# Optimization experiments

Hardware: AMD Instinct MI355X
Metric: run time of the kernel (lower is better)

## Reference

```python
import jax, jax.numpy as jnp
import numpy as np

N = 131072        # total nodes (2048 graphs * MAX_N)
E = 1048576       # edges
F_IN = 128        # g_feature_n
INT_D = 256       # int_d
H1, C1 = 8, 8     # gl: heads, head_d
C2 = 256          # gl2: out channels, heads=1
MAX_N = 64
NEG_SLOPE = 0.2
BN_EPS = 1e-5


def _gat_conv(x, src, dst, W, att_src, att_dst, bias, heads, out_c):
    """PyG GATConv (concat=True), self-loops already appended to src/dst."""
    n = x.shape[0]
    h = (x @ W.T).reshape(n, heads, out_c)                  # [N,H,C]
    a_s = jnp.sum(h * att_src, axis=-1)                     # [N,H]
    a_d = jnp.sum(h * att_dst, axis=-1)                     # [N,H]
    alpha = jax.nn.leaky_relu(a_s[src] + a_d[dst], NEG_SLOPE)  # [E',H]
    amax = jax.ops.segment_max(alpha, dst, num_segments=n)  # stable segment softmax
    e = jnp.exp(alpha - amax[dst])
    denom = jax.ops.segment_sum(e, dst, num_segments=n)
    w = e / (denom[dst] + 1e-16)                            # [E',H]
    out = jax.ops.segment_sum(h[src] * w[..., None], dst, num_segments=n)
    return out.reshape(n, heads * out_c) + bias


def setup_inputs() -> dict:
    key = jax.random.key(0)
    ks = jax.random.split(key, 20)
    s = 0.1
    return {
        "x": jax.random.normal(ks[0], (N, F_IN), jnp.float32),
        "edge_index": jax.random.randint(ks[1], (2, E), 0, N, jnp.int64),
        # lin_embed
        "We": jax.random.normal(ks[2], (INT_D, F_IN), jnp.float32) * s,
        "be": jnp.zeros((INT_D,), jnp.float32),
        # batchnorm (eval mode, running stats)
        "bn_gamma": jnp.ones((INT_D,), jnp.float32),
        "bn_beta": jnp.zeros((INT_D,), jnp.float32),
        "bn_mean": jax.random.normal(ks[3], (INT_D,), jnp.float32) * 0.01,
        "bn_var": jax.random.uniform(ks[4], (INT_D,), jnp.float32, 0.5, 1.5),
        # gl: GATConv(INT_D -> C1, heads=H1)
        "W1": jax.random.normal(ks[5], (H1 * C1, INT_D), jnp.float32) * s,
        "as1": jax.random.normal(ks[6], (1, H1, C1), jnp.float32) * s,
        "ad1": jax.random.normal(ks[7], (1, H1, C1), jnp.float32) * s,
        "b1": jnp.zeros((H1 * C1,), jnp.float32),
        # gl2: GATConv(H1*C1 -> C2, heads=1)
        "W2": jax.random.normal(ks[8], (C2, H1 * C1), jnp.float32) * s,
        "as2": jax.random.normal(ks[9], (1, 1, C2), jnp.float32) * s,
        "ad2": jax.random.normal(ks[10], (1, 1, C2), jnp.float32) * s,
        "b2": jnp.zeros((C2,), jnp.float32),
        # lin_out
        "Wo": jax.random.normal(ks[11], (1, INT_D), jnp.float32) * s,
        "bo": jnp.zeros((1,), jnp.float32),
    }


def reference(x, edge_index, We, be, bn_gamma, bn_beta, bn_mean, bn_var,
              W1, as1, ad1, b1, W2, as2, ad2, b2, Wo, bo):
    n = x.shape[0]
    loops = jnp.arange(n)
    src = jnp.concatenate([edge_index[0], loops])  # add_self_loops=True (PyG default)
    dst = jnp.concatenate([edge_index[1], loops])

    h = x @ We.T + be
    h = (h - bn_mean) * jax.lax.rsqrt(bn_var + BN_EPS) * bn_gamma + bn_beta

    h = jax.nn.elu(_gat_conv(h, src, dst, W1, as1, ad1, b1, H1, C1))
    h = _gat_conv(h, src, dst, W2, as2, ad2, b2, 1, C2)

    mu = (h @ Wo.T + bo).reshape(-1, MAX_N, 1)
    return mu, jnp.zeros_like(mu)
```

## Files before the change

### kernel.cpp

```cpp
#include <hip/hip_runtime.h>
#include <hip/hip_bf16.h>

#define NN 131072
#define NE 1048576
#define CAP 48
#define INVLN2 1.44269504088896341f

typedef unsigned short u16;
typedef unsigned int u32;

__device__ __forceinline__ float bf2f(u16 u) {
  return __uint_as_float(((unsigned int)u) << 16);
}
__device__ __forceinline__ u16 f2bf(float f) {
  unsigned int u = __float_as_uint(f);
  unsigned int r = ((u >> 16) & 1u) + 0x7fffu;
  return (u16)((u + r) >> 16);
}
__device__ __forceinline__ float leakyf(float x) { return x >= 0.f ? x : 0.2f * x; }

constexpr size_t OFF_H1   = 0;
constexpr size_t OFF_AS1N = 16777216;
constexpr size_t OFF_AD1N = 20971520;
constexpr size_t OFF_ZS   = 25165824;
constexpr size_t OFF_AD2N = 26214400;
constexpr size_t OFF_CNT  = 26738688;
constexpr size_t OFF_COL  = 27262976;
constexpr size_t OFF_MP   = 52428800;
constexpr size_t OFF_C1AC = 52469760;
constexpr size_t OFF_V2   = 52470064;

__global__ __launch_bounds__(256) void fill1_fold_kernel(
    const int* __restrict__ ei, int* cnt, int* colv, const float* W1, const float* We,
    const float* be, const float* bng, const float* bnb, const float* bnm,
    const float* bnv, const float* as1, const float* ad1, const float* W2,
    const float* as2, const float* ad2, const float* Wo, const float* b2,
    const float* bo, float* MP, float* c1ac, float* v2) {
  int b = blockIdx.x;
  int t = threadIdx.x;
  if (b < 2048) {
    int p = b & 7;
    int base = (b >> 3) * 2048;
    int dsts[8], srcs[8];
#pragma unroll
    for (int j = 0; j < 8; ++j) {
      dsts[j] = ei[NE + base + t + 256 * j];
      srcs[j] = ei[base + t + 256 * j];
    }
#pragma unroll
    for (int j = 0; j < 8; ++j) {
      if ((dsts[j] >> 14) == p) {
        int slot = atomicAdd(&cnt[dsts[j]], 1);
        colv[dsts[j] * CAP + slot] = srcs[j];
      }
    }
  } else if (b < 2088) {
    __shared__ float L[2][256];
    int mrow = b - 2048;
    int r0 = mrow * 2;
    int lr = t >> 7, k = t & 127;
    float sgc = bng[t] * rsqrtf(bnv[t] + 1e-5f);
#pragma unroll
    for (int q = 0; q < 2; ++q) {
      int r = r0 + q;
      float coef;
      if (r < 64) {
        coef = W1[r * 256 + t];
      } else if (r < 72) {
        int h = r - 64;
        coef = 0.f;
#pragma unroll
        for (int j = 0; j < 8; ++j) coef += as1[h * 8 + j] * W1[(h * 8 + j) * 256 + t];
        coef *= INVLN2;
      } else {
        int h = r - 72;
        coef = 0.f;
#pragma unroll
        for (int j = 0; j < 8; ++j) coef += ad1[h * 8 + j] * W1[(h * 8 + j) * 256 + t];
        coef *= INVLN2;
      }
      L[q][t] = coef * sgc;
    }
    __syncthreads();
    float acc = 0.f;
    for (int c = 0; c < 256; ++c) acc += L[lr][c] * We[c * 128 + k];
    MP[(size_t)(r0 + lr) * 128 + k] = acc;
  } else if (b == 2088) {
    __shared__ float ofs[256];
    __shared__ float c1l[64];
    float sgc = bng[t] * rsqrtf(bnv[t] + 1e-5f);
    ofs[t] = (be[t] - bnm[t]) * sgc + bnb[t];
    __syncthreads();
    if (t < 64) {
      float a = 0.f;
      for (int c = 0; c < 256; ++c) a += W1[t * 256 + c] * ofs[c];
      c1ac[t] = a;
      c1l[t] = a;
    }
    __syncthreads();
    if (t < 8) {
      float s = 0.f;
#pragma unroll
      for (int j = 0; j < 8; ++j) s += c1l[t * 8 + j] * (as1[t * 8 + j] + ad1[t * 8 + j]);
      c1ac[64 + t] = s * INVLN2;
    }
  } else {
    __shared__ float pa[4][64], pd[4][64], pz[4][64];
    int k = t & 63, part = t >> 6;
    float a = 0.f, d = 0.f, z = 0.f;
    for (int c = part * 64; c < part * 64 + 64; ++c) {
      float w = W2[c * 64 + k];
      a += as2[c] * w;
      d += ad2[c] * w;
      z += Wo[c] * w;
    }
    pa[part][k] = a;
    pd[part][k] = d;
    pz[part][k] = z;
    __syncthreads();
    if (t < 64) {
      v2[t]       = (pa[0][t] + pa[1][t] + pa[2][t] + pa[3][t]) * INVLN2;
      v2[64 + t]  = (pd[0][t] + pd[1][t] + pd[2][t] + pd[3][t]) * INVLN2;
      v2[128 + t] = pz[0][t] + pz[1][t] + pz[2][t] + pz[3][t];
      float cc = b2[t] * Wo[t] + b2[64 + t] * Wo[64 + t] +
                 b2[128 + t] * Wo[128 + t] + b2[192 + t] * Wo[192 + t];
      for (int o = 1; o < 64; o <<= 1) cc += __shfl_xor(cc, o);
      if (t == 0) v2[192] = cc + bo[0];
    }
  }
}

__global__ __launch_bounds__(256) void gemm_fill2_kernel(const float* __restrict__ x,
                                                         const float* __restrict__ MP,
                                                         u16* __restrict__ h1,
                                                         float* __restrict__ as1n,
                                                         float* __restrict__ ad1n,
                                                         const int* __restrict__ ei,
                                                         int* cnt, int* colv) {
  __shared__ float4 sM[80 * 32];
  int b = blockIdx.x;
  int t = threadIdx.x;
  if (b >= 512) {
    int fb = b - 512;
    int p = fb & 7;
    int base = NE / 2 + (fb >> 3) * 2048;
    int dsts[8], srcs[8];
#pragma unroll
    for (int j = 0; j < 8; ++j) {
      dsts[j] = ei[NE + base + t + 256 * j];
      srcs[j] = ei[base + t + 256 * j];
    }
#pragma unroll
    for (int j = 0; j < 8; ++j) {
      if ((dsts[j] >> 14) == p) {
        int slot = atomicAdd(&cnt[dsts[j]], 1);
        colv[dsts[j] * CAP + slot] = srcs[j];
      }
    }
    return;
  }
  int lane = t & 63, wv = t >> 6;
  const float4* MPv = (const float4*)MP;
  for (int i = t; i < 2560; i += 256) sM[i] = MPv[i];
  __syncthreads();
  int c0 = (wv & 1) * 40;
  size_t r0 = (size_t)b * 256 + (wv >> 1) * 128 + lane;
  const float4* x0 = (const float4*)(x + r0 * 128);
  const float4* x1 = (const float4*)(x + (r0 + 64) * 128);
  float a0[40], a1[40];
#pragma unroll
  for (int c = 0; c < 40; ++c) { a0[c] = 0.f; a1[c] = 0.f; }
  for (int q = 0; q < 32; ++q) {
    float4 cx0 = x0[q];
    float4 cx1 = x1[q];
    const float4* mp = sM + c0 * 32 + q;
#pragma unroll
    for (int c = 0; c < 40; ++c) {
      float4 B = mp[c * 32];
      a0[c] += cx0.x * B.x; a0[c] += cx0.y * B.y;
      a0[c] += cx0.z * B.z; a0[c] += cx0.w * B.w;
      a1[c] += cx1.x * B.x; a1[c] += cx1.y * B.y;
      a1[c] += cx1.z * B.z; a1[c] += cx1.w * B.w;
    }
  }
#pragma unroll
  for (int rr = 0; rr < 2; ++rr) {
    size_t row = r0 + rr * 64;
    if (c0 == 0) {
      u32 ux[20];
#pragma unroll
      for (int j = 0; j < 20; ++j) {
        float lo = rr ? a1[2 * j] : a0[2 * j];
        float hi = rr ? a1[2 * j + 1] : a0[2 * j + 1];
        ux[j] = (u32)f2bf(lo) | ((u32)f2bf(hi) << 16);
      }
      uint4* dst = (uint4*)(h1 + row * 64);
#pragma unroll
      for (int j = 0; j < 5; ++j)
        dst[j] = make_uint4(ux[4 * j], ux[4 * j + 1], ux[4 * j + 2], ux[4 * j + 3]);
    } else {
      u32 ux[12];
#pragma unroll
      for (int j = 0; j < 12; ++j) {
        float lo = rr ? a1[2 * j] : a0[2 * j];
        float hi = rr ? a1[2 * j + 1] : a0[2 * j + 1];
        ux[j] = (u32)f2bf(lo) | ((u32)f2bf(hi) << 16);
      }
      uint4* dst = (uint4*)(h1 + row * 64 + 40);
#pragma unroll
      for (int j = 0; j < 3; ++j)
        dst[j] = make_uint4(ux[4 * j], ux[4 * j + 1], ux[4 * j + 2], ux[4 * j + 3]);
      float4* as4 = (float4*)(as1n + row * 8);
      float4* ad4 = (float4*)(ad1n + row * 8);
      if (rr == 0) {
        as4[0] = make_float4(a0[24], a0[25], a0[26], a0[27]);
        as4[1] = make_float4(a0[28], a0[29], a0[30], a0[31]);
        ad4[0] = make_float4(a0[32], a0[33], a0[34], a0[35]);
        ad4[1] = make_float4(a0[36], a0[37], a0[38], a0[39]);
      } else {
        as4[0] = make_float4(a1[24], a1[25], a1[26], a1[27]);
        as4[1] = make_float4(a1[28], a1[29], a1[30], a1[31]);
        ad4[0] = make_float4(a1[32], a1[33], a1[34], a1[35]);
        ad4[1] = make_float4(a1[36], a1[37], a1[38], a1[39]);
      }
    }
  }
}

__global__ __launch_bounds__(256) void gat1_agg_kernel(const int* __restrict__ cnt,
                                                       const int* __restrict__ colv,
                                                       const float* __restrict__ as1n,
                                                       const float* __restrict__ ad1n,
                                                       const u16* __restrict__ h1,
                                                       const float* b1,
                                                       const float* __restrict__ c1ac,
                                                       const float* v2,
                                                       float2* zs, float* ad2n) {
  __shared__ float wlds[4][64];
  __shared__ int slds[4][8];
  int t = threadIdx.x, lane = t & 63, wv = t >> 6;
  int n = blockIdx.x * 4 + wv;
  int m = lane & 31;
  int half = lane >> 5;
  int hh = m >> 2;
  int h1i = lane & 7;
  int e8 = lane >> 3;
  int start = n * CAP;
  int end = start + cnt[n];
  const char* h1b = (const char*)h1;
  float adh = ad1n[(size_t)n * 8 + hh] + c1ac[64 + hh];
  float ws = exp2f(leakyf(as1n[(size_t)n * 8 + hh] + adh));
  u32 sv = *(const u32*)(h1b + ((size_t)n << 7) + m * 4);
  float wsel = half ? 0.f : ws;
  float acc0 = wsel * __uint_as_float(sv << 16);
  float acc1 = wsel * __uint_as_float(sv & 0xffff0000u);
  float dd = 0.f;
  float ad_p1 = ad1n[(size_t)n * 8 + h1i] + c1ac[64 + h1i];
  for (int base = start; base < end; base += 8) {
    int mm = end - base;
    if (mm > 8) mm = 8;
    int eidx = base + e8;
    int ecl = (eidx < end) ? eidx : (end - 1);
    int s = colv[ecl];
    float w = (e8 < mm) ? exp2f(leakyf(as1n[(size_t)s * 8 + h1i] + ad_p1)) : 0.f;
    if (h1i == 0) slds[wv][e8] = s;
    wlds[wv][lane] = w;
#pragma unroll
    for (int i = 0; i < 4; ++i) {
      int e = 2 * i + half;
      float wi = wlds[wv][e * 8 + hh];
      int si = slds[wv][e];
      u32 v = *(const u32*)(h1b + ((size_t)si << 7) + m * 4);
      dd += wi;
      acc0 += wi * __uint_as_float(v << 16);
      acc1 += wi * __uint_as_float(v & 0xffff0000u);
    }
  }
  acc0 += __shfl_xor(acc0, 32);
  acc1 += __shfl_xor(acc1, 32);
  dd += __shfl_xor(dd, 32);
  float denom = ws + dd;
  float dinv = __builtin_amdgcn_rcpf(denom + 1e-16f);
  float2 c1p = ((const float2*)c1ac)[m];
  float2 b1p = ((const float2*)b1)[m];
  float v0 = acc0 * dinv + c1p.x + b1p.x;
  float v1 = acc1 * dinv + c1p.y + b1p.y;
  v0 = v0 > 0.f ? v0 : __expf(v0) - 1.f;
  v1 = v1 > 0.f ? v1 : __expf(v1) - 1.f;
  float2 vap = ((const float2*)v2)[m];
  float2 vdp = ((const float2*)(v2 + 64))[m];
  float2 vzp = ((const float2*)(v2 + 128))[m];
  float p0 = v0 * vap.x + v1 * vap.y;
  float p1 = v0 * vdp.x + v1 * vdp.y;
  float p2 = v0 * vzp.x + v1 * vzp.y;
  for (int o = 1; o < 32; o <<= 1) {
    p0 += __shfl_xor(p0, o);
    p1 += __shfl_xor(p1, o);
    p2 += __shfl_xor(p2, o);
  }
  if (lane == 0) {
    zs[n] = make_float2(p0, p2);
    ad2n[n] = p1;
  }
}

__global__ __launch_bounds__(256) void gat2_kernel(const int* __restrict__ cnt,
                                                   const int* __restrict__ colv,
                                                   const float2* __restrict__ zs,
                                                   const float* __restrict__ ad2n,
                                                   const float* v2, float* out) {
  int t = threadIdx.x;
  int g = t & 7;
  int n = blockIdx.x * 32 + (t >> 3);
  int start = n * CAP;
  int end = start + cnt[n];
  float ad = ad2n[n];
  float num = 0.f, den = 0.f;
  for (int e = start + g; e < end; e += 8) {
    int s = colv[e];
    float2 tt = zs[s];
    float wi = exp2f(leakyf(tt.x + ad));
    num += wi * tt.y;
    den += wi;
  }
  if (g == 0) {
    float2 self = zs[n];
    float w = exp2f(leakyf(self.x + ad));
    num += w * self.y;
    den += w;
  }
  num += __shfl_xor(num, 1); den += __shfl_xor(den, 1);
  num += __shfl_xor(num, 2); den += __shfl_xor(den, 2);
  num += __shfl_xor(num, 4); den += __shfl_xor(den, 4);
  if (g == 0) {
    out[n] = num * __builtin_amdgcn_rcpf(den + 1e-16f) + v2[192];
    out[NN + n] = 0.f;
  }
}

extern "C" void kernel_launch(void* const* d_in, const int* in_sizes, int n_in,
                              void* d_out, int out_size, void* d_ws, size_t ws_size,
                              hipStream_t stream) {
  const float* x   = (const float*)d_in[0];
  const int*   ei  = (const int*)d_in[1];
  const float* We  = (const float*)d_in[2];
  const float* be  = (const float*)d_in[3];
  const float* bng = (const float*)d_in[4];
  const float* bnb = (const float*)d_in[5];
  const float* bnm = (const float*)d_in[6];
  const float* bnv = (const float*)d_in[7];
  const float* W1  = (const float*)d_in[8];
  const float* as1 = (const float*)d_in[9];
  const float* ad1 = (const float*)d_in[10];
  const float* b1  = (const float*)d_in[11];
  const float* W2  = (const float*)d_in[12];
  const float* as2 = (const float*)d_in[13];
  const float* ad2 = (const float*)d_in[14];
  const float* b2  = (const float*)d_in[15];
  const float* Wo  = (const float*)d_in[16];
  const float* bo  = (const float*)d_in[17];
  float* out = (float*)d_out;

  char* ws = (char*)d_ws;
  u16*    h1   = (u16*)(ws + OFF_H1);
  float*  as1n = (float*)(ws + OFF_AS1N);
  float*  ad1n = (float*)(ws + OFF_AD1N);
  float2* zs   = (float2*)(ws + OFF_ZS);
  float*  ad2n = (float*)(ws + OFF_AD2N);
  int*    cnt  = (int*)(ws + OFF_CNT);
  int*    colv = (int*)(ws + OFF_COL);
  float*  MP   = (float*)(ws + OFF_MP);
  float*  c1ac = (float*)(ws + OFF_C1AC);
  float*  v2   = (float*)(ws + OFF_V2);

  hipMemsetAsync(cnt, 0, NN * sizeof(int), stream);
  fill1_fold_kernel<<<2090, 256, 0, stream>>>(ei, cnt, colv, W1, We, be, bng, bnb,
                                              bnm, bnv, as1, ad1, W2, as2, ad2, Wo,
                                              b2, bo, MP, c1ac, v2);
  gemm_fill2_kernel<<<2560, 256, 0, stream>>>(x, MP, h1, as1n, ad1n, ei, cnt, colv);
  gat1_agg_kernel<<<NN / 4, 256, 0, stream>>>(cnt, colv, as1n, ad1n, h1, b1, c1ac, v2, zs, ad2n);
  gat2_kernel<<<NN / 32, 256, 0, stream>>>(cnt, colv, zs, ad2n, v2, out);
}
```

Measured before the change: 187.3 us.

## Split GEMM K-dimension across 4 lanes per row with shuffle reduction

The fused GEMM now assigns one row to four lanes, each covering a quarter of the K dimension for all 80 output columns, then combines the partial sums with xor shuffles. Before, each thread owned two full rows and 40 columns. The goal is 4x more GEMM blocks (2048 instead of 512) with coalesced x loads, raising parallelism and memory-level concurrency. The cost is 80 accumulators per thread, which raises register pressure, plus 160 shuffles per thread. LDS traffic per FMA also goes up, since each B value now feeds only one row.

```diff
diff --git a/kernel.cpp b/kernel.cpp
--- a/kernel.cpp
+++ b/kernel.cpp
@@ -140,8 +140,8 @@
   __shared__ float4 sM[80 * 32];
   int b = blockIdx.x;
   int t = threadIdx.x;
-  if (b >= 512) {
-    int fb = b - 512;
+  if (b >= 2048) {
+    int fb = b - 2048;
     int p = fb & 7;
     int base = NE / 2 + (fb >> 3) * 2048;
     int dsts[8], srcs[8];
@@ -163,67 +163,43 @@
   const float4* MPv = (const float4*)MP;
   for (int i = t; i < 2560; i += 256) sM[i] = MPv[i];
   __syncthreads();
-  int c0 = (wv & 1) * 40;
-  size_t r0 = (size_t)b * 256 + (wv >> 1) * 128 + lane;
-  const float4* x0 = (const float4*)(x + r0 * 128);
-  const float4* x1 = (const float4*)(x + (r0 + 64) * 128);
-  float a0[40], a1[40];
-#pragma unroll
-  for (int c = 0; c < 40; ++c) { a0[c] = 0.f; a1[c] = 0.f; }
-  for (int q = 0; q < 32; ++q) {
-    float4 cx0 = x0[q];
-    float4 cx1 = x1[q];
-    const float4* mp = sM + c0 * 32 + q;
-#pragma unroll
-    for (int c = 0; c < 40; ++c) {
+  int r = lane >> 2, qk = lane & 3;
+  size_t row = (size_t)b * 64 + wv * 16 + r;
+  const float4* xr = (const float4*)(x + row * 128);
+  float acc[80];
+#pragma unroll
+  for (int c = 0; c < 80; ++c) acc[c] = 0.f;
+  for (int q = 0; q < 8; ++q) {
+    float4 xv = xr[q * 4 + qk];
+    const float4* mp = sM + q * 4 + qk;
+#pragma unroll
+    for (int c = 0; c < 80; ++c) {
       float4 B = mp[c * 32];
-      a0[c] += cx0.x * B.x; a0[c] += cx0.y * B.y;
-      a0[c] += cx0.z * B.z; a0[c] += cx0.w * B.w;
-      a1[c] += cx1.x * B.x; a1[c] += cx1.y * B.y;
-      a1[c] += cx1.z * B.z; a1[c] += cx1.w * B.w;
-    }
-  }
-#pragma unroll
-  for (int rr = 0; rr < 2; ++rr) {
-    size_t row = r0 + rr * 64;
-    if (c0 == 0) {
-      u32 ux[20];
-#pragma unroll
-      for (int j = 0; j < 20; ++j) {
-        float lo = rr ? a1[2 * j] : a0[2 * j];
-        float hi = rr ? a1[2 * j + 1] : a0[2 * j + 1];
-        ux[j] = (u32)f2bf(lo) | ((u32)f2bf(hi) << 16);
-      }
-      uint4* dst = (uint4*)(h1 + row * 64);
-#pragma unroll
-      for (int j = 0; j < 5; ++j)
-        dst[j] = make_uint4(ux[4 * j], ux[4 * j + 1], ux[4 * j + 2], ux[4 * j + 3]);
-    } else {
-      u32 ux[12];
-#pragma unroll
-      for (int j = 0; j < 12; ++j) {
-        float lo = rr ? a1[2 * j] : a0[2 * j];
-        float hi = rr ? a1[2 * j + 1] : a0[2 * j + 1];
-        ux[j] = (u32)f2bf(lo) | ((u32)f2bf(hi) << 16);
-      }
-      uint4* dst = (uint4*)(h1 + row * 64 + 40);
-#pragma unroll
-      for (int j = 0; j < 3; ++j)
-        dst[j] = make_uint4(ux[4 * j], ux[4 * j + 1], ux[4 * j + 2], ux[4 * j + 3]);
-      float4* as4 = (float4*)(as1n + row * 8);
-      float4* ad4 = (float4*)(ad1n + row * 8);
-      if (rr == 0) {
-        as4[0] = make_float4(a0[24], a0[25], a0[26], a0[27]);
-        as4[1] = make_float4(a0[28], a0[29], a0[30], a0[31]);
-        ad4[0] = make_float4(a0[32], a0[33], a0[34], a0[35]);
-        ad4[1] = make_float4(a0[36], a0[37], a0[38], a0[39]);
-      } else {
-        as4[0] = make_float4(a1[24], a1[25], a1[26], a1[27]);
-        as4[1] = make_float4(a1[28], a1[29], a1[30], a1[31]);
-        ad4[0] = make_float4(a1[32], a1[33], a1[34], a1[35]);
-        ad4[1] = make_float4(a1[36], a1[37], a1[38], a1[39]);
-      }
-    }
+      acc[c] += xv.x * B.x;
+      acc[c] += xv.y * B.y;
+      acc[c] += xv.z * B.z;
+      acc[c] += xv.w * B.w;
+    }
+  }
+#pragma unroll
+  for (int c = 0; c < 80; ++c) {
+    acc[c] += __shfl_xor(acc[c], 1);
+    acc[c] += __shfl_xor(acc[c], 2);
+  }
+#pragma unroll
+  for (int jj = 0; jj < 2; ++jj) {
+    int j = qk + jj * 4;
+    u32 u0 = (u32)f2bf(acc[8 * j + 0]) | ((u32)f2bf(acc[8 * j + 1]) << 16);
+    u32 u1 = (u32)f2bf(acc[8 * j + 2]) | ((u32)f2bf(acc[8 * j + 3]) << 16);
+    u32 u2 = (u32)f2bf(acc[8 * j + 4]) | ((u32)f2bf(acc[8 * j + 5]) << 16);
+    u32 u3 = (u32)f2bf(acc[8 * j + 6]) | ((u32)f2bf(acc[8 * j + 7]) << 16);
+    ((uint4*)(h1 + row * 64))[j] = make_uint4(u0, u1, u2, u3);
+  }
+  {
+    int base4 = 64 + qk * 4;
+    float4 vv = make_float4(acc[base4], acc[base4 + 1], acc[base4 + 2], acc[base4 + 3]);
+    float* dst = (qk < 2) ? (as1n + row * 8 + qk * 4) : (ad1n + row * 8 + (qk - 2) * 4);
+    *(float4*)dst = vv;
   }
 }
 
@@ -377,7 +353,7 @@
   fill1_fold_kernel<<<2090, 256, 0, stream>>>(ei, cnt, colv, W1, We, be, bng, bnb,
                                               bnm, bnv, as1, ad1, W2, as2, ad2, Wo,
                                               b2, bo, MP, c1ac, v2);
-  gemm_fill2_kernel<<<2560, 256, 0, stream>>>(x, MP, h1, as1n, ad1n, ei, cnt, colv);
+  gemm_fill2_kernel<<<4096, 256, 0, stream>>>(x, MP, h1, as1n, ad1n, ei, cnt, colv);
   gat1_agg_kernel<<<NN / 4, 256, 0, stream>>>(cnt, colv, as1n, ad1n, h1, b1, c1ac, v2, zs, ad2n);
   gat2_kernel<<<NN / 32, 256, 0, stream>>>(cnt, colv, zs, ad2n, v2, out);
 }
```

After: 248.6 us. 32.7% more time.
